# Optimization experiments

Hardware: AMD Instinct MI355X
Metric: run time of the kernel (lower is better)

The kernel has to match this reference:

```python
import jax, jax.numpy as jnp
import numpy as np
import math

B, T, C, H, E = 1, 384, 512, 8, 16
D = C // H

def layer_norm(x, w, b, eps=1e-5):
    mu = jnp.mean(x, axis=-1, keepdims=True)
    var = jnp.mean(jnp.square(x - mu), axis=-1, keepdims=True)
    return (x - mu) * jax.lax.rsqrt(var + eps) * w + b

def setup_inputs() -> dict:
    key = jax.random.key(0)
    ks = jax.random.split(key, 12)
    s = 0.02
    return {
        'x': jax.random.normal(ks[0], (B, T, C), jnp.float32),
        'bias_matrix': jax.random.randint(ks[1], (B, T, T), 0, E, jnp.int32),
        'ln1_w': jnp.ones((C,), jnp.float32),
        'ln1_b': jnp.zeros((C,), jnp.float32),
        'w_attn_w': jax.random.normal(ks[2], (3 * C, C), jnp.float32) * s,
        'w_attn_b': jnp.zeros((3 * C,), jnp.float32),
        'w_proj_w': jax.random.normal(ks[3], (C, C), jnp.float32) * s,
        'w_proj_b': jnp.zeros((C,), jnp.float32),
        'attn_bias_emb': jax.random.normal(ks[4], (E, H), jnp.float32) * s,
        'edge_emb': jax.random.normal(ks[5], (E, C), jnp.float32) * s,
        'w_edge_k_w': jax.random.normal(ks[6], (C, C), jnp.float32) * s,
        'w_edge_k_b': jnp.zeros((C,), jnp.float32),
        'w_edge_v_w': jax.random.normal(ks[7], (C, C), jnp.float32) * s,
        'w_edge_v_b': jnp.zeros((C,), jnp.float32),
        'ln2_w': jnp.ones((C,), jnp.float32),
        'ln2_b': jnp.zeros((C,), jnp.float32),
        'c_fc_w': jax.random.normal(ks[8], (4 * C, C), jnp.float32) * s,
        'c_fc_b': jnp.zeros((4 * C,), jnp.float32),
        'c_proj_w': jax.random.normal(ks[9], (C, 4 * C), jnp.float32) * s,
        'c_proj_b': jnp.zeros((C,), jnp.float32),
    }

def reference(x, bias_matrix, ln1_w, ln1_b, w_attn_w, w_attn_b, w_proj_w, w_proj_b,
              attn_bias_emb, edge_emb, w_edge_k_w, w_edge_k_b, w_edge_v_w, w_edge_v_b,
              ln2_w, ln2_b, c_fc_w, c_fc_b, c_proj_w, c_proj_b):
    # --- attention branch ---
    h = layer_norm(x, ln1_w, ln1_b)
    qkv = h @ w_attn_w.T + w_attn_b                      # (B,T,3C)
    q, k, v = jnp.split(qkv, 3, axis=-1)
    q = q.reshape(B, T, H, D).transpose(0, 2, 1, 3)      # (B,H,T,D)
    k = k.reshape(B, T, H, D).transpose(0, 2, 1, 3)
    v = v.reshape(B, T, H, D).transpose(0, 2, 1, 3)
    scale = math.sqrt(D)

    ee = edge_emb[bias_matrix]                           # (B,T,T,C)
    e_k = (ee @ w_edge_k_w.T + w_edge_k_b).reshape(B, T, T, H, D)
    # score[b,h,i,j] = sum_d q[b,h,i,d] * k[b,h,j,d] * e_k[b,i,j,h,d]
    scores = jnp.einsum('bhid,bhjd,bijhd->bhij', q, k, e_k) / scale

    mask = jnp.tril(jnp.ones((T, T), bool))              # causal, diag included
    scores = jnp.where(mask, scores, -jnp.inf)
    ab = attn_bias_emb[bias_matrix].transpose(0, 3, 1, 2)  # (B,H,T,T)
    ab = jnp.where(mask, ab, 0.0)
    attn = jax.nn.softmax(scores + ab, axis=-1)

    e_v = (ee @ w_edge_v_w.T + w_edge_v_b).reshape(B, T, T, H, D)
    # y[b,h,i,d] = sum_j attn[b,h,i,j] * v[b,h,j,d] * e_v[b,i,j,h,d]
    y = jnp.einsum('bhij,bhjd,bijhd->bhid', attn, v, e_v)
    y = y.transpose(0, 2, 1, 3).reshape(B, T, C)
    y = y @ w_proj_w.T + w_proj_b
    x = x + y

    # --- MLP branch ---
    h2 = layer_norm(x, ln2_w, ln2_b)
    h2 = jax.nn.gelu(h2 @ c_fc_w.T + c_fc_b, approximate=False)
    x = x + (h2 @ c_proj_w.T + c_proj_b)
    return x
```

## Files before the change

kernel.cpp:

```cpp
#include <hip/hip_runtime.h>
#include <math.h>

#define TT 384
#define CC 512
#define HH 8
#define EE 16

typedef __bf16 bf16_t;
typedef __bf16 bf16x8 __attribute__((ext_vector_type(8)));
typedef __bf16 bf16x4v __attribute__((ext_vector_type(4)));
typedef float f32x4 __attribute__((ext_vector_type(4)));

__device__ __forceinline__ float wave_reduce_sum(float v) {
#pragma unroll
  for (int off = 32; off >= 1; off >>= 1) v += __shfl_xor(v, off, 64);
  return v;
}

__device__ __forceinline__ void wrow_unit(const float* __restrict__ wr,
                                          const float* __restrict__ g,
                                          const float* __restrict__ bb,
                                          float extra_c, bf16_t* __restrict__ orow,
                                          float* __restrict__ s1p,
                                          float* __restrict__ cp, int lane) {
  const float* p = wr + lane * 8;
  f32x4 w0 = *(const f32x4*)p, w1 = *(const f32x4*)(p + 4);
  f32x4 g0 = *(const f32x4*)(g + lane * 8), g1 = *(const f32x4*)(g + lane * 8 + 4);
  f32x4 b0 = *(const f32x4*)(bb + lane * 8), b1 = *(const f32x4*)(bb + lane * 8 + 4);
  f32x4 p0 = w0 * g0, p1 = w1 * g1;
  bf16x8 o;
  o[0] = (bf16_t)p0.x; o[1] = (bf16_t)p0.y; o[2] = (bf16_t)p0.z; o[3] = (bf16_t)p0.w;
  o[4] = (bf16_t)p1.x; o[5] = (bf16_t)p1.y; o[6] = (bf16_t)p1.z; o[7] = (bf16_t)p1.w;
  *(bf16x8*)(orow + lane * 8) = o;
  float s1 = p0.x + p0.y + p0.z + p0.w + p1.x + p1.y + p1.z + p1.w;
  float c = w0.x * b0.x + w0.y * b0.y + w0.z * b0.z + w0.w * b0.w +
            w1.x * b1.x + w1.y * b1.y + w1.z * b1.z + w1.w * b1.w;
  s1 = wave_reduce_sum(s1);
  c = wave_reduce_sum(c);
  if (lane == 0) { *s1p = s1; *cp = c + extra_c; }
}

struct PrepX {
  const float *eemb, *wekw, *wekb, *wevw, *wevb;
  const float *ln2w, *ln2b, *cfcw, *cfcb;
  const float *wproj, *wcproj;
  float *ektab, *evtab, *s1f, *cf;
  bf16_t *wfc_bf, *wproj_bf, *wcproj_bf;
};

__device__ void prep_unit(int u, const PrepX& X, int tid) {
  int lane = tid & 63, wave = tid >> 6;
  if (u < 256) {
    int wid = u * 4 + wave;
    int gbase = wid * 16;
    int table = gbase >> 13;
    int e = (gbase >> 9) & 15;
    int c0 = gbase & 511;
    const float* er = X.eemb + e * 512 + lane * 8;
    f32x4 ea = *(const f32x4*)er;
    f32x4 eb = *(const f32x4*)(er + 4);
    const float* wbase = table ? X.wevw : X.wekw;
    const float* bbase = table ? X.wevb : X.wekb;
    float* obase = (table ? X.evtab : X.ektab) + e * 512;
#pragma unroll
    for (int o = 0; o < 16; o++) {
      int c = c0 + o;
      const float* wr = wbase + (size_t)c * 512 + lane * 8;
      f32x4 wa = *(const f32x4*)wr;
      f32x4 wb = *(const f32x4*)(wr + 4);
      float acc = ea.x * wa.x + ea.y * wa.y + ea.z * wa.z + ea.w * wa.w +
                  eb.x * wb.x + eb.y * wb.y + eb.z * wb.z + eb.w * wb.w;
      acc = wave_reduce_sum(acc);
      if (lane == 0) obase[c] = acc + bbase[c];
    }
  } else if (u < 768) {
    int n = (u - 256) * 4 + wave;
    wrow_unit(X.cfcw + (size_t)n * 512, X.ln2w, X.ln2b, X.cfcb[n],
              X.wfc_bf + (size_t)n * 512, X.s1f + n, X.cf + n, lane);
  } else if (u < 1024) {
    int base = (u - 768) * 1024;
    for (int t = tid; t < 1024; t += 256) {
      f32x4 a = *((const f32x4*)X.wcproj + base + t);
      bf16x4v o;
      o[0] = (bf16_t)a.x; o[1] = (bf16_t)a.y; o[2] = (bf16_t)a.z; o[3] = (bf16_t)a.w;
      *((bf16x4v*)X.wcproj_bf + base + t) = o;
    }
  } else if (u < 1088) {
    int base = (u - 1024) * 1024;
    for (int t = tid; t < 1024; t += 256) {
      f32x4 a = *((const f32x4*)X.wproj + base + t);
      bf16x4v o;
      o[0] = (bf16_t)a.x; o[1] = (bf16_t)a.y; o[2] = (bf16_t)a.z; o[3] = (bf16_t)a.w;
      *((bf16x4v*)X.wproj_bf + base + t) = o;
    }
  }
}

struct PreArgs {
  const float *x, *ln1w, *ln1b, *wattn, *wattnb;
  float *xmu, *xrs, *x1s1, *x1s2, *s1q, *cq;
  bf16_t* wqkv_bf;
};

__global__ __launch_bounds__(256) void pre_k(PreArgs P) {
  int b = blockIdx.x, tid = threadIdx.x, lane = tid & 63, wave = tid >> 6;
  if (b < 384) {
    int n = b * 4 + wave;
    wrow_unit(P.wattn + (size_t)n * 512, P.ln1w, P.ln1b, P.wattnb[n],
              P.wqkv_bf + (size_t)n * 512, P.s1q + n, P.cq + n, lane);
  } else if (b < 480) {
    int r = (b - 384) * 4 + wave;
    const float* xr = P.x + (size_t)r * 512 + lane * 8;
    f32x4 a = *(const f32x4*)xr, c = *(const f32x4*)(xr + 4);
    float s = a.x + a.y + a.z + a.w + c.x + c.y + c.z + c.w;
    float q = a.x * a.x + a.y * a.y + a.z * a.z + a.w * a.w +
              c.x * c.x + c.y * c.y + c.z * c.z + c.w * c.w;
    s = wave_reduce_sum(s);
    q = wave_reduce_sum(q);
    if (lane == 0) {
      float mu = s * (1.0f / 512.0f);
      float var = q * (1.0f / 512.0f) - mu * mu;
      P.xmu[r] = mu;
      P.xrs[r] = rsqrtf(var + 1e-5f);
    }
  } else {
    for (int i = tid; i < 384; i += 256) { P.x1s1[i] = 0.f; P.x1s2[i] = 0.f; }
  }
}

template <int MODE>
__global__ __launch_bounds__(256) void gemm_k(
    const void* __restrict__ Aptr, const bf16_t* __restrict__ Wb,
    const float* __restrict__ e0, const float* __restrict__ e1,
    const float* __restrict__ e2, const float* __restrict__ e3,
    const float* __restrict__ res, void* __restrict__ out,
    float* __restrict__ st1, float* __restrict__ st2, int N, int K, PrepX X) {
  constexpr bool AF32 = (MODE == 0 || MODE == 2);
  constexpr int AW = AF32 ? 2 : 1;
  __shared__ float part[4][32][32];
  int tid = threadIdx.x;
  if (MODE == 0 && blockIdx.y >= 12) {
    prep_unit((blockIdx.y - 12) * gridDim.x + blockIdx.x, X, tid);
    return;
  }
  int lane = tid & 63, wave = tid >> 6;
  int m0 = blockIdx.y * 32, n0 = blockIdx.x * 32;
  int r16 = lane & 15, quad = lane >> 4;
  int kchunk = K >> 2, k0 = wave * kchunk;

  f32x4 acc[2][2];
  f32x4 zero = {0.f, 0.f, 0.f, 0.f};
#pragma unroll
  for (int i = 0; i < 2; i++)
#pragma unroll
    for (int j = 0; j < 2; j++) acc[i][j] = zero;

  const float* Af = (const float*)Aptr + (size_t)(m0 + r16) * K + k0 + quad * 8;
  const bf16_t* Ab = (const bf16_t*)Aptr + (size_t)(m0 + r16) * K + k0 + quad * 8;
  const bf16_t* Wp = Wb + (size_t)(n0 + r16) * K + k0 + quad * 8;

  for (int kb0 = 0; kb0 < kchunk; kb0 += 128) {
    uint4 araw[4][2][AW];
    uint4 braw[4][2];
#pragma unroll
    for (int u = 0; u < 4; u++) {
      int kb = kb0 + u * 32;
#pragma unroll
      for (int t = 0; t < 2; t++) {
        if (AF32) {
          araw[u][t][0] = *(const uint4*)(Af + (size_t)t * 16 * K + kb);
          araw[u][t][1] = *(const uint4*)(Af + (size_t)t * 16 * K + kb + 4);
        } else {
          araw[u][t][0] = *(const uint4*)(Ab + (size_t)t * 16 * K + kb);
        }
        braw[u][t] = *(const uint4*)(Wp + (size_t)t * 16 * K + kb);
      }
    }
#pragma unroll
    for (int u = 0; u < 4; u++) {
      bf16x8 af[2], bfr[2];
#pragma unroll
      for (int t = 0; t < 2; t++) {
        if (AF32) {
          f32x4 a = *reinterpret_cast<const f32x4*>(&araw[u][t][0]);
          f32x4 c = *reinterpret_cast<const f32x4*>(&araw[u][t][1]);
          af[t][0] = (bf16_t)a.x; af[t][1] = (bf16_t)a.y;
          af[t][2] = (bf16_t)a.z; af[t][3] = (bf16_t)a.w;
          af[t][4] = (bf16_t)c.x; af[t][5] = (bf16_t)c.y;
          af[t][6] = (bf16_t)c.z; af[t][7] = (bf16_t)c.w;
        } else {
          af[t] = *reinterpret_cast<const bf16x8*>(&araw[u][t][0]);
        }
        bfr[t] = *reinterpret_cast<const bf16x8*>(&braw[u][t]);
      }
#pragma unroll
      for (int i = 0; i < 2; i++)
#pragma unroll
        for (int j = 0; j < 2; j++)
          acc[i][j] = __builtin_amdgcn_mfma_f32_16x16x32_bf16(af[i], bfr[j],
                                                              acc[i][j], 0, 0, 0);
    }
  }

#pragma unroll
  for (int i = 0; i < 2; i++)
#pragma unroll
    for (int j = 0; j < 2; j++)
#pragma unroll
      for (int r = 0; r < 4; r++)
        part[wave][i * 16 + quad * 4 + r][j * 16 + r16] = acc[i][j][r];
  __syncthreads();

  int row = tid >> 3, c4 = (tid & 7) * 4;
  f32x4 v = *(const f32x4*)&part[0][row][c4];
  v += *(const f32x4*)&part[1][row][c4];
  v += *(const f32x4*)&part[2][row][c4];
  v += *(const f32x4*)&part[3][row][c4];
  int grow = m0 + row, gcol = n0 + c4;

  if (MODE == 0 || MODE == 2) {
    float mu, rs;
    if (MODE == 0) {
      mu = e0[grow]; rs = e1[grow];
    } else {
      float S = e0[grow], Q = e1[grow];
      mu = S * (1.0f / 512.0f);
      float var = Q * (1.0f / 512.0f) - mu * mu;
      rs = rsqrtf(var + 1e-5f);
    }
    f32x4 s1v = *(const f32x4*)(e2 + gcol);
    f32x4 ccv = *(const f32x4*)(e3 + gcol);
#pragma unroll
    for (int t = 0; t < 4; t++) {
      float x = rs * (v[t] - mu * s1v[t]) + ccv[t];
      if (MODE == 2) x = 0.5f * x * (1.0f + erff(x * 0.70710678118654752f));
      v[t] = x;
    }
    bf16x4v o;
#pragma unroll
    for (int t = 0; t < 4; t++) o[t] = (bf16_t)v[t];
    *(bf16x4v*)((bf16_t*)out + (size_t)grow * N + gcol) = o;
  } else {
    v += *(const f32x4*)(e2 + gcol);
    v += *(const f32x4*)(res + (size_t)grow * N + gcol);
    *(f32x4*)((float*)out + (size_t)grow * N + gcol) = v;
    if (MODE == 1) {
      float sv = v.x + v.y + v.z + v.w;
      float qv = v.x * v.x + v.y * v.y + v.z * v.z + v.w * v.w;
      sv += __shfl_down(sv, 4, 8); qv += __shfl_down(qv, 4, 8);
      sv += __shfl_down(sv, 2, 8); qv += __shfl_down(qv, 2, 8);
      sv += __shfl_down(sv, 1, 8); qv += __shfl_down(qv, 1, 8);
      if ((tid & 7) == 0) {
        atomicAdd(st1 + grow, sv);
        atomicAdd(st2 + grow, qv);
      }
    }
  }
}

__global__ __launch_bounds__(256) void attn_k(
    const bf16_t* __restrict__ qkv, const int* __restrict__ bias_matrix,
    const float* __restrict__ attn_bias_emb, const float* __restrict__ ek_tab,
    const float* __restrict__ ev_tab, bf16_t* __restrict__ ybuf) {
  __shared__ float s[TT];
  __shared__ int ebuf[TT];
  __shared__ float qe[EE][68];
  __shared__ float evh[EE * 64];
  __shared__ float red[4 * 64];
  __shared__ float absh[EE];
  __shared__ float scr[4];

  int i = blockIdx.x, h = blockIdx.y;
  int tid = threadIdx.x, lane = tid & 63, wave = tid >> 6;
  int n = i + 1;

  for (int j = tid; j < n; j += 256) ebuf[j] = bias_matrix[i * TT + j];
  if (tid < EE) absh[tid] = attn_bias_emb[tid * HH + h];
  for (int idx = tid; idx < EE * 64; idx += 256) {
    int e = idx >> 6, d = idx & 63;
    float qv = (float)qkv[(size_t)i * 1536 + h * 64 + d];
    qe[e][d] = qv * ek_tab[e * 512 + h * 64 + d];
    evh[idx] = ev_tab[e * 512 + h * 64 + d];
  }
  __syncthreads();

  float ls = 0.0f;
  for (int jl = tid; jl < n; jl += 256) {
    int e = ebuf[jl];
    const uint4* kp = (const uint4*)(qkv + (size_t)jl * 1536 + 512 + h * 64);
    uint4 kr[8];
#pragma unroll
    for (int dg = 0; dg < 8; dg++) kr[dg] = kp[dg];
    float acc = 0.f;
#pragma unroll
    for (int dg = 0; dg < 8; dg++) {
      bf16x8 kv = *reinterpret_cast<const bf16x8*>(&kr[dg]);
      f32x4 qa = *(const f32x4*)&qe[e][dg * 8];
      f32x4 qb = *(const f32x4*)&qe[e][dg * 8 + 4];
      acc += (float)kv[0] * qa.x + (float)kv[1] * qa.y + (float)kv[2] * qa.z +
             (float)kv[3] * qa.w + (float)kv[4] * qb.x + (float)kv[5] * qb.y +
             (float)kv[6] * qb.z + (float)kv[7] * qb.w;
    }
    float p = __expf(acc * 0.125f + absh[e]);
    s[jl] = p;
    ls += p;
  }
  ls = wave_reduce_sum(ls);
  if (lane == 0) scr[wave] = ls;
  __syncthreads();
  float inv = 1.0f / (scr[0] + scr[1] + scr[2] + scr[3]);

  float acc = 0.0f;
  int j = wave;
  for (; j + 4 < n; j += 8) {
    int e0 = ebuf[j], e1 = ebuf[j + 4];
    float p0 = s[j], p1 = s[j + 4];
    float v0 = (float)qkv[(size_t)j * 1536 + 1024 + h * 64 + lane];
    float v1 = (float)qkv[(size_t)(j + 4) * 1536 + 1024 + h * 64 + lane];
    acc += p0 * v0 * evh[e0 * 64 + lane] + p1 * v1 * evh[e1 * 64 + lane];
  }
  for (; j < n; j += 4) {
    int e = ebuf[j];
    float vv = (float)qkv[(size_t)j * 1536 + 1024 + h * 64 + lane];
    acc += s[j] * vv * evh[e * 64 + lane];
  }
  red[wave * 64 + lane] = acc;
  __syncthreads();
  if (tid < 64) {
    float y = (red[tid] + red[64 + tid] + red[128 + tid] + red[192 + tid]) * inv;
    ybuf[(size_t)i * CC + h * 64 + tid] = (bf16_t)y;
  }
}

extern "C" void kernel_launch(void* const* d_in, const int* in_sizes, int n_in,
                              void* d_out, int out_size, void* d_ws,
                              size_t ws_size, hipStream_t stream) {
  const float* x = (const float*)d_in[0];
  const int* bias_mat = (const int*)d_in[1];

  char* wp = (char*)d_ws;
  float* ektab = (float*)wp;  wp += 16 * 512 * 4;
  float* evtab = (float*)wp;  wp += 16 * 512 * 4;
  float* xmu = (float*)wp;    wp += 384 * 4;
  float* xrs = (float*)wp;    wp += 384 * 4;
  float* x1s1 = (float*)wp;   wp += 384 * 4;
  float* x1s2 = (float*)wp;   wp += 384 * 4;
  float* s1q = (float*)wp;    wp += 1536 * 4;
  float* cq = (float*)wp;     wp += 1536 * 4;
  float* s1f = (float*)wp;    wp += 2048 * 4;
  float* cf = (float*)wp;     wp += 2048 * 4;
  float* x1 = (float*)wp;     wp += 384 * 512 * 4;
  bf16_t* wqkv_bf = (bf16_t*)wp;   wp += 1536 * 512 * 2;
  bf16_t* wfc_bf = (bf16_t*)wp;    wp += 2048 * 512 * 2;
  bf16_t* wproj_bf = (bf16_t*)wp;  wp += 512 * 512 * 2;
  bf16_t* wcproj_bf = (bf16_t*)wp; wp += 512 * 2048 * 2;
  bf16_t* qkv = (bf16_t*)wp;  wp += 384 * 1536 * 2;
  bf16_t* ybuf = (bf16_t*)wp; wp += 384 * 512 * 2;
  bf16_t* gbuf = (bf16_t*)wp; wp += 384 * 2048 * 2;

  PreArgs P;
  P.x = x;
  P.ln1w = (const float*)d_in[2];
  P.ln1b = (const float*)d_in[3];
  P.wattn = (const float*)d_in[4];
  P.wattnb = (const float*)d_in[5];
  P.xmu = xmu; P.xrs = xrs; P.x1s1 = x1s1; P.x1s2 = x1s2;
  P.s1q = s1q; P.cq = cq; P.wqkv_bf = wqkv_bf;

  PrepX X;
  X.eemb = (const float*)d_in[9];
  X.wekw = (const float*)d_in[10];
  X.wekb = (const float*)d_in[11];
  X.wevw = (const float*)d_in[12];
  X.wevb = (const float*)d_in[13];
  X.ln2w = (const float*)d_in[14];
  X.ln2b = (const float*)d_in[15];
  X.cfcw = (const float*)d_in[16];
  X.cfcb = (const float*)d_in[17];
  X.wproj = (const float*)d_in[6];
  X.wcproj = (const float*)d_in[18];
  X.ektab = ektab; X.evtab = evtab; X.s1f = s1f; X.cf = cf;
  X.wfc_bf = wfc_bf; X.wproj_bf = wproj_bf; X.wcproj_bf = wcproj_bf;

  pre_k<<<481, 256, 0, stream>>>(P);
  gemm_k<0><<<dim3(48, 35), 256, 0, stream>>>(x, wqkv_bf, xmu, xrs, s1q, cq,
                                              nullptr, qkv, nullptr, nullptr,
                                              1536, 512, X);
  attn_k<<<dim3(TT, HH), 256, 0, stream>>>(qkv, bias_mat,
                                           (const float*)d_in[8], ektab, evtab,
                                           ybuf);
  gemm_k<1><<<dim3(16, 12), 256, 0, stream>>>(
      ybuf, wproj_bf, nullptr, nullptr, (const float*)d_in[7], nullptr, x, x1,
      x1s1, x1s2, 512, 512, X);
  gemm_k<2><<<dim3(64, 12), 256, 0, stream>>>(x1, wfc_bf, x1s1, x1s2, s1f, cf,
                                              nullptr, gbuf, nullptr, nullptr,
                                              2048, 512, X);
  gemm_k<3><<<dim3(16, 12), 256, 0, stream>>>(
      gbuf, wcproj_bf, nullptr, nullptr, (const float*)d_in[19], nullptr, x1,
      d_out, nullptr, nullptr, 512, 2048, X);
}
```

Measured before the change: 174.8 us.

## Fuse LN1 stats and QKV weight prep into the QKV GEMM kernel

Measured after the change: 173.6 us (median of 2 runs). No clear change (-0.7%).

```diff
diff --git a/kernel.cpp b/kernel.cpp
--- a/kernel.cpp
+++ b/kernel.cpp
@@ -44,7 +44,7 @@
   const float *eemb, *wekw, *wekb, *wevw, *wevb;
   const float *ln2w, *ln2b, *cfcw, *cfcb;
   const float *wproj, *wcproj;
-  float *ektab, *evtab, *s1f, *cf;
+  float *ektab, *evtab, *s1f, *cf, *x1s1, *x1s2;
   bf16_t *wfc_bf, *wproj_bf, *wcproj_bf;
 };
 
@@ -93,39 +93,139 @@
       o[0] = (bf16_t)a.x; o[1] = (bf16_t)a.y; o[2] = (bf16_t)a.z; o[3] = (bf16_t)a.w;
       *((bf16x4v*)X.wproj_bf + base + t) = o;
     }
-  }
-}
-
-struct PreArgs {
-  const float *x, *ln1w, *ln1b, *wattn, *wattnb;
-  float *xmu, *xrs, *x1s1, *x1s2, *s1q, *cq;
-  bf16_t* wqkv_bf;
-};
-
-__global__ __launch_bounds__(256) void pre_k(PreArgs P) {
-  int b = blockIdx.x, tid = threadIdx.x, lane = tid & 63, wave = tid >> 6;
-  if (b < 384) {
-    int n = b * 4 + wave;
-    wrow_unit(P.wattn + (size_t)n * 512, P.ln1w, P.ln1b, P.wattnb[n],
-              P.wqkv_bf + (size_t)n * 512, P.s1q + n, P.cq + n, lane);
-  } else if (b < 480) {
-    int r = (b - 384) * 4 + wave;
-    const float* xr = P.x + (size_t)r * 512 + lane * 8;
-    f32x4 a = *(const f32x4*)xr, c = *(const f32x4*)(xr + 4);
-    float s = a.x + a.y + a.z + a.w + c.x + c.y + c.z + c.w;
-    float q = a.x * a.x + a.y * a.y + a.z * a.z + a.w * a.w +
-              c.x * c.x + c.y * c.y + c.z * c.z + c.w * c.w;
-    s = wave_reduce_sum(s);
-    q = wave_reduce_sum(q);
-    if (lane == 0) {
-      float mu = s * (1.0f / 512.0f);
-      float var = q * (1.0f / 512.0f) - mu * mu;
-      P.xmu[r] = mu;
-      P.xrs[r] = rsqrtf(var + 1e-5f);
-    }
-  } else {
-    for (int i = tid; i < 384; i += 256) { P.x1s1[i] = 0.f; P.x1s2[i] = 0.f; }
-  }
+  } else if (u == 1088) {
+    for (int i = tid; i < 384; i += 256) { X.x1s1[i] = 0.f; X.x1s2[i] = 0.f; }
+  }
+}
+
+__global__ __launch_bounds__(256) void qkv_k(
+    const float* __restrict__ x, const float* __restrict__ wattn,
+    const float* __restrict__ ln1w, const float* __restrict__ ln1b,
+    const float* __restrict__ wattnb, bf16_t* __restrict__ out, PrepX X) {
+  int tid = threadIdx.x;
+  if (blockIdx.y >= 12) {
+    prep_unit((blockIdx.y - 12) * gridDim.x + blockIdx.x, X, tid);
+    return;
+  }
+  __shared__ float part[4][32][32];
+  __shared__ float rst[2][4][32];
+  __shared__ float wst[2][4][32];
+  int lane = tid & 63, wave = tid >> 6;
+  int m0 = blockIdx.y * 32, n0 = blockIdx.x * 32;
+  int r16 = lane & 15, quad = lane >> 4;
+  int k0 = wave * 128;
+
+  f32x4 acc[2][2];
+  f32x4 zero = {0.f, 0.f, 0.f, 0.f};
+#pragma unroll
+  for (int i = 0; i < 2; i++)
+#pragma unroll
+    for (int j = 0; j < 2; j++) acc[i][j] = zero;
+
+  const float* Af = x + (size_t)(m0 + r16) * 512 + k0 + quad * 8;
+  const float* Wf = wattn + (size_t)(n0 + r16) * 512 + k0 + quad * 8;
+  const float* gp = ln1w + k0 + quad * 8;
+  const float* bp = ln1b + k0 + quad * 8;
+
+  float sx[2] = {0.f, 0.f}, sxx[2] = {0.f, 0.f};
+  float s1[2] = {0.f, 0.f}, cc[2] = {0.f, 0.f};
+
+  for (int kb0 = 0; kb0 < 128; kb0 += 64) {
+    uint4 araw[2][2][2], wraw[2][2][2];
+#pragma unroll
+    for (int u = 0; u < 2; u++) {
+      int kb = kb0 + u * 32;
+#pragma unroll
+      for (int t = 0; t < 2; t++) {
+        araw[u][t][0] = *(const uint4*)(Af + (size_t)t * 16 * 512 + kb);
+        araw[u][t][1] = *(const uint4*)(Af + (size_t)t * 16 * 512 + kb + 4);
+        wraw[u][t][0] = *(const uint4*)(Wf + (size_t)t * 16 * 512 + kb);
+        wraw[u][t][1] = *(const uint4*)(Wf + (size_t)t * 16 * 512 + kb + 4);
+      }
+    }
+#pragma unroll
+    for (int u = 0; u < 2; u++) {
+      int kb = kb0 + u * 32;
+      f32x4 g0 = *(const f32x4*)(gp + kb), g1 = *(const f32x4*)(gp + kb + 4);
+      f32x4 b0 = *(const f32x4*)(bp + kb), b1 = *(const f32x4*)(bp + kb + 4);
+      bf16x8 af[2], bfr[2];
+#pragma unroll
+      for (int t = 0; t < 2; t++) {
+        f32x4 a0 = *reinterpret_cast<const f32x4*>(&araw[u][t][0]);
+        f32x4 a1 = *reinterpret_cast<const f32x4*>(&araw[u][t][1]);
+        af[t][0] = (bf16_t)a0.x; af[t][1] = (bf16_t)a0.y;
+        af[t][2] = (bf16_t)a0.z; af[t][3] = (bf16_t)a0.w;
+        af[t][4] = (bf16_t)a1.x; af[t][5] = (bf16_t)a1.y;
+        af[t][6] = (bf16_t)a1.z; af[t][7] = (bf16_t)a1.w;
+        sx[t] += a0.x + a0.y + a0.z + a0.w + a1.x + a1.y + a1.z + a1.w;
+        sxx[t] += a0.x * a0.x + a0.y * a0.y + a0.z * a0.z + a0.w * a0.w +
+                  a1.x * a1.x + a1.y * a1.y + a1.z * a1.z + a1.w * a1.w;
+        f32x4 w0 = *reinterpret_cast<const f32x4*>(&wraw[u][t][0]);
+        f32x4 w1 = *reinterpret_cast<const f32x4*>(&wraw[u][t][1]);
+        f32x4 p0 = w0 * g0, p1 = w1 * g1;
+        bfr[t][0] = (bf16_t)p0.x; bfr[t][1] = (bf16_t)p0.y;
+        bfr[t][2] = (bf16_t)p0.z; bfr[t][3] = (bf16_t)p0.w;
+        bfr[t][4] = (bf16_t)p1.x; bfr[t][5] = (bf16_t)p1.y;
+        bfr[t][6] = (bf16_t)p1.z; bfr[t][7] = (bf16_t)p1.w;
+        s1[t] += p0.x + p0.y + p0.z + p0.w + p1.x + p1.y + p1.z + p1.w;
+        cc[t] += w0.x * b0.x + w0.y * b0.y + w0.z * b0.z + w0.w * b0.w +
+                 w1.x * b1.x + w1.y * b1.y + w1.z * b1.z + w1.w * b1.w;
+      }
+#pragma unroll
+      for (int i = 0; i < 2; i++)
+#pragma unroll
+        for (int j = 0; j < 2; j++)
+          acc[i][j] = __builtin_amdgcn_mfma_f32_16x16x32_bf16(af[i], bfr[j],
+                                                              acc[i][j], 0, 0, 0);
+    }
+  }
+
+#pragma unroll
+  for (int t = 0; t < 2; t++) {
+    sx[t] += __shfl_xor(sx[t], 16, 64);  sx[t] += __shfl_xor(sx[t], 32, 64);
+    sxx[t] += __shfl_xor(sxx[t], 16, 64); sxx[t] += __shfl_xor(sxx[t], 32, 64);
+    s1[t] += __shfl_xor(s1[t], 16, 64);  s1[t] += __shfl_xor(s1[t], 32, 64);
+    cc[t] += __shfl_xor(cc[t], 16, 64);  cc[t] += __shfl_xor(cc[t], 32, 64);
+  }
+  if (quad == 0) {
+#pragma unroll
+    for (int t = 0; t < 2; t++) {
+      rst[0][wave][t * 16 + r16] = sx[t];
+      rst[1][wave][t * 16 + r16] = sxx[t];
+      wst[0][wave][t * 16 + r16] = s1[t];
+      wst[1][wave][t * 16 + r16] = cc[t];
+    }
+  }
+#pragma unroll
+  for (int i = 0; i < 2; i++)
+#pragma unroll
+    for (int j = 0; j < 2; j++)
+#pragma unroll
+      for (int r = 0; r < 4; r++)
+        part[wave][i * 16 + quad * 4 + r][j * 16 + r16] = acc[i][j][r];
+  __syncthreads();
+
+  int row = tid >> 3, c4 = (tid & 7) * 4;
+  f32x4 v = *(const f32x4*)&part[0][row][c4];
+  v += *(const f32x4*)&part[1][row][c4];
+  v += *(const f32x4*)&part[2][row][c4];
+  v += *(const f32x4*)&part[3][row][c4];
+  float sxt = rst[0][0][row] + rst[0][1][row] + rst[0][2][row] + rst[0][3][row];
+  float sxxt = rst[1][0][row] + rst[1][1][row] + rst[1][2][row] + rst[1][3][row];
+  float mu = sxt * (1.0f / 512.0f);
+  float var = sxxt * (1.0f / 512.0f) - mu * mu;
+  float rs = rsqrtf(var + 1e-5f);
+  int grow = m0 + row, gcol = n0 + c4;
+  bf16x4v o;
+#pragma unroll
+  for (int t = 0; t < 4; t++) {
+    int cl = c4 + t;
+    float s1v = wst[0][0][cl] + wst[0][1][cl] + wst[0][2][cl] + wst[0][3][cl];
+    float ccv = wst[1][0][cl] + wst[1][1][cl] + wst[1][2][cl] + wst[1][3][cl] +
+                wattnb[n0 + cl];
+    o[t] = (bf16_t)(rs * (v[t] - mu * s1v) + ccv);
+  }
+  *(bf16x4v*)(out + (size_t)grow * 1536 + gcol) = o;
 }
 
 template <int MODE>
@@ -134,15 +234,11 @@
     const float* __restrict__ e0, const float* __restrict__ e1,
     const float* __restrict__ e2, const float* __restrict__ e3,
     const float* __restrict__ res, void* __restrict__ out,
-    float* __restrict__ st1, float* __restrict__ st2, int N, int K, PrepX X) {
-  constexpr bool AF32 = (MODE == 0 || MODE == 2);
+    float* __restrict__ st1, float* __restrict__ st2, int N, int K) {
+  constexpr bool AF32 = (MODE == 2);
   constexpr int AW = AF32 ? 2 : 1;
   __shared__ float part[4][32][32];
   int tid = threadIdx.x;
-  if (MODE == 0 && blockIdx.y >= 12) {
-    prep_unit((blockIdx.y - 12) * gridDim.x + blockIdx.x, X, tid);
-    return;
-  }
   int lane = tid & 63, wave = tid >> 6;
   int m0 = blockIdx.y * 32, n0 = blockIdx.x * 32;
   int r16 = lane & 15, quad = lane >> 4;
@@ -218,27 +314,20 @@
   v += *(const f32x4*)&part[3][row][c4];
   int grow = m0 + row, gcol = n0 + c4;
 
-  if (MODE == 0 || MODE == 2) {
-    float mu, rs;
-    if (MODE == 0) {
-      mu = e0[grow]; rs = e1[grow];
-    } else {
-      float S = e0[grow], Q = e1[grow];
-      mu = S * (1.0f / 512.0f);
-      float var = Q * (1.0f / 512.0f) - mu * mu;
-      rs = rsqrtf(var + 1e-5f);
-    }
+  if (MODE == 2) {
+    float S = e0[grow], Q = e1[grow];
+    float mu = S * (1.0f / 512.0f);
+    float var = Q * (1.0f / 512.0f) - mu * mu;
+    float rs = rsqrtf(var + 1e-5f);
     f32x4 s1v = *(const f32x4*)(e2 + gcol);
     f32x4 ccv = *(const f32x4*)(e3 + gcol);
+    bf16x4v o;
 #pragma unroll
     for (int t = 0; t < 4; t++) {
-      float x = rs * (v[t] - mu * s1v[t]) + ccv[t];
-      if (MODE == 2) x = 0.5f * x * (1.0f + erff(x * 0.70710678118654752f));
-      v[t] = x;
-    }
-    bf16x4v o;
-#pragma unroll
-    for (int t = 0; t < 4; t++) o[t] = (bf16_t)v[t];
+      float xg = rs * (v[t] - mu * s1v[t]) + ccv[t];
+      xg = 0.5f * xg * (1.0f + erff(xg * 0.70710678118654752f));
+      o[t] = (bf16_t)xg;
+    }
     *(bf16x4v*)((bf16_t*)out + (size_t)grow * N + gcol) = o;
   } else {
     v += *(const f32x4*)(e2 + gcol);
@@ -341,31 +430,17 @@
   char* wp = (char*)d_ws;
   float* ektab = (float*)wp;  wp += 16 * 512 * 4;
   float* evtab = (float*)wp;  wp += 16 * 512 * 4;
-  float* xmu = (float*)wp;    wp += 384 * 4;
-  float* xrs = (float*)wp;    wp += 384 * 4;
   float* x1s1 = (float*)wp;   wp += 384 * 4;
   float* x1s2 = (float*)wp;   wp += 384 * 4;
-  float* s1q = (float*)wp;    wp += 1536 * 4;
-  float* cq = (float*)wp;     wp += 1536 * 4;
   float* s1f = (float*)wp;    wp += 2048 * 4;
   float* cf = (float*)wp;     wp += 2048 * 4;
   float* x1 = (float*)wp;     wp += 384 * 512 * 4;
-  bf16_t* wqkv_bf = (bf16_t*)wp;   wp += 1536 * 512 * 2;
   bf16_t* wfc_bf = (bf16_t*)wp;    wp += 2048 * 512 * 2;
   bf16_t* wproj_bf = (bf16_t*)wp;  wp += 512 * 512 * 2;
   bf16_t* wcproj_bf = (bf16_t*)wp; wp += 512 * 2048 * 2;
   bf16_t* qkv = (bf16_t*)wp;  wp += 384 * 1536 * 2;
   bf16_t* ybuf = (bf16_t*)wp; wp += 384 * 512 * 2;
   bf16_t* gbuf = (bf16_t*)wp; wp += 384 * 2048 * 2;
-
-  PreArgs P;
-  P.x = x;
-  P.ln1w = (const float*)d_in[2];
-  P.ln1b = (const float*)d_in[3];
-  P.wattn = (const float*)d_in[4];
-  P.wattnb = (const float*)d_in[5];
-  P.xmu = xmu; P.xrs = xrs; P.x1s1 = x1s1; P.x1s2 = x1s2;
-  P.s1q = s1q; P.cq = cq; P.wqkv_bf = wqkv_bf;
 
   PrepX X;
   X.eemb = (const float*)d_in[9];
@@ -380,22 +455,22 @@
   X.wproj = (const float*)d_in[6];
   X.wcproj = (const float*)d_in[18];
   X.ektab = ektab; X.evtab = evtab; X.s1f = s1f; X.cf = cf;
+  X.x1s1 = x1s1; X.x1s2 = x1s2;
   X.wfc_bf = wfc_bf; X.wproj_bf = wproj_bf; X.wcproj_bf = wcproj_bf;
 
-  pre_k<<<481, 256, 0, stream>>>(P);
-  gemm_k<0><<<dim3(48, 35), 256, 0, stream>>>(x, wqkv_bf, xmu, xrs, s1q, cq,
-                                              nullptr, qkv, nullptr, nullptr,
-                                              1536, 512, X);
+  qkv_k<<<dim3(48, 35), 256, 0, stream>>>(
+      x, (const float*)d_in[4], (const float*)d_in[2], (const float*)d_in[3],
+      (const float*)d_in[5], qkv, X);
   attn_k<<<dim3(TT, HH), 256, 0, stream>>>(qkv, bias_mat,
                                            (const float*)d_in[8], ektab, evtab,
                                            ybuf);
   gemm_k<1><<<dim3(16, 12), 256, 0, stream>>>(
       ybuf, wproj_bf, nullptr, nullptr, (const float*)d_in[7], nullptr, x, x1,
-      x1s1, x1s2, 512, 512, X);
+      x1s1, x1s2, 512, 512);
   gemm_k<2><<<dim3(64, 12), 256, 0, stream>>>(x1, wfc_bf, x1s1, x1s2, s1f, cf,
                                               nullptr, gbuf, nullptr, nullptr,
-                                              2048, 512, X);
+                                              2048, 512);
   gemm_k<3><<<dim3(16, 12), 256, 0, stream>>>(
       gbuf, wcproj_bf, nullptr, nullptr, (const float*)d_in[19], nullptr, x1,
-      d_out, nullptr, nullptr, 512, 2048, X);
-}
+      d_out, nullptr, nullptr, 512, 2048);
+}
```
